# Performance work log

Hardware: AMD Instinct MI355X
Metric: run time of the kernel (lower is better)

The kernel has to match this reference:

```python
import jax, jax.numpy as jnp
import numpy as np

B, DIM, HEADS, HD, H, W = 1, 256, 8, 32, 64, 64
MLP = int(DIM * 4.0)
EPS = 1e-5


def _ln(x, g, b):
    # LayerNorm over channel dim of NCHW (torch applies it on NHWC last dim)
    mu = x.mean(axis=1, keepdims=True)
    var = ((x - mu) ** 2).mean(axis=1, keepdims=True)
    return (x - mu) / jnp.sqrt(var + EPS) * g[None, :, None, None] + b[None, :, None, None]


def _c1(x, w, b):
    # 1x1 conv: w is [out, in]
    return jnp.einsum('bchw,oc->bohw', x, w) + b[None, :, None, None]


def _c3(x, w, b):
    y = jax.lax.conv_general_dilated(x, w, (1, 1), ((1, 1), (1, 1)),
                                     dimension_numbers=('NCHW', 'OIHW', 'NCHW'))
    return y + b[None, :, None, None]


def setup_inputs() -> dict:
    key = jax.random.key(0)
    ks = jax.random.split(key, 16)
    init = lambda k, s: jax.random.normal(k, s, jnp.float32) * 0.02
    d = {}
    d['rgb_feat'] = jax.random.normal(ks[0], (B, DIM, H, W), jnp.float32)
    d['dpt_feat'] = jax.random.normal(ks[1], (B, DIM, H, W), jnp.float32)
    d['x_dpt'] = jax.random.normal(ks[2], (B, 1, 1024, 1024), jnp.float32)
    d['wq'] = init(ks[3], (DIM, DIM)); d['bq'] = jnp.zeros((DIM,), jnp.float32)
    d['wk'] = init(ks[4], (DIM, DIM)); d['bk'] = jnp.zeros((DIM,), jnp.float32)
    d['wv'] = init(ks[5], (DIM, DIM)); d['bv'] = jnp.zeros((DIM,), jnp.float32)
    d['wo'] = init(ks[6], (DIM, DIM)); d['bo'] = jnp.zeros((DIM,), jnp.float32)
    d['g_rgb'] = jnp.ones((DIM,), jnp.float32); d['b_rgb'] = jnp.zeros((DIM,), jnp.float32)
    d['g_dpt'] = jnp.ones((DIM,), jnp.float32); d['b_dpt'] = jnp.zeros((DIM,), jnp.float32)
    d['g1'] = jnp.ones((DIM,), jnp.float32); d['b1'] = jnp.zeros((DIM,), jnp.float32)
    d['g2'] = jnp.ones((DIM,), jnp.float32); d['b2'] = jnp.zeros((DIM,), jnp.float32)
    d['w_mlp1'] = init(ks[7], (MLP, DIM)); d['b_mlp1'] = jnp.zeros((MLP,), jnp.float32)
    d['w_mlp2'] = init(ks[8], (DIM, MLP)); d['b_mlp2'] = jnp.zeros((DIM,), jnp.float32)
    d['w_de1'] = init(ks[9], (DIM, 1, 3, 3)); d['b_de1'] = jnp.zeros((DIM,), jnp.float32)
    d['w_de2'] = init(ks[10], (DIM, DIM)); d['b_de2'] = jnp.zeros((DIM,), jnp.float32)
    d['pos_emb'] = init(ks[11], (1, DIM, 1, 1))
    d['scale'] = jnp.sqrt(jnp.float32(HD))
    return d


def reference(rgb_feat, dpt_feat, x_dpt, wq, bq, wk, bk, wv, bv, wo, bo,
              g_rgb, b_rgb, g_dpt, b_dpt, g1, b1, g2, b2,
              w_mlp1, b_mlp1, w_mlp2, b_mlp2, w_de1, b_de1, w_de2, b_de2,
              pos_emb, scale):
    Bn, C, Hh, Ww = rgb_feat.shape
    n = Hh * Ww
    rgb_ln = _ln(rgb_feat, g_rgb, b_rgb)
    dpt_ln = _ln(dpt_feat, g_dpt, b_dpt)
    # depth positional embedding: bilinear downsample (align_corners=False) + conv3x3 + relu + conv1x1
    xd = jax.image.resize(x_dpt, (Bn, 1, Hh, Ww), method='bilinear', antialias=False)
    pe = _c1(jax.nn.relu(_c3(xd, w_de1, b_de1)), w_de2, b_de2)
    rgb_ln = rgb_ln + pos_emb + pe
    dpt_ln = dpt_ln + pos_emb + pe
    # QKV as [B, heads, head_dim, N]
    q = _c1(rgb_ln, wq, bq).reshape(Bn, HEADS, HD, n)
    k = _c1(dpt_ln, wk, bk).reshape(Bn, HEADS, HD, n)
    v = _c1(dpt_ln, wv, bv).reshape(Bn, HEADS, HD, n)
    scores = jnp.einsum('bhdn,bhdm->bhnm', q, k) / scale
    attn = jax.nn.softmax(scores, axis=-1)  # dropout is identity in eval
    fused = jnp.einsum('bhnm,bhdm->bhdn', attn, v).reshape(Bn, C, Hh, Ww)
    out = _c1(fused, wo, bo) + rgb_feat
    out_ln = _ln(out, g1, b1)
    h = jax.nn.gelu(_c1(out_ln, w_mlp1, b_mlp1), approximate=False)
    mlp_out = _c1(h, w_mlp2, b_mlp2)
    out2 = mlp_out + out_ln
    return _ln(out2, g2, b2)
```

## Files before the change

kernel.cpp:

```cpp
#include <hip/hip_runtime.h>
#include <hip/hip_bf16.h>
#include <math.h>

constexpr int NTOK = 4096;
constexpr int CDIM = 256;
constexpr int MLPD = 1024;
constexpr int SPLIT = 4;
constexpr float EPS_LN = 1e-5f;

typedef __attribute__((ext_vector_type(8))) short bf16x8;
typedef __attribute__((ext_vector_type(4))) float floatx4;
typedef unsigned short u16;
typedef unsigned int u32;

__device__ __forceinline__ u16 f2bf(float x) {
    union { float f; u32 u; } v; v.f = x;
    u32 r = v.u + 0x7fff + ((v.u >> 16) & 1);
    return (u16)(r >> 16);
}
__device__ __forceinline__ float bf2f(u16 u) {
    union { u32 i; float f; } v; v.i = ((u32)u) << 16; return v.f;
}
__device__ __forceinline__ u32 pkbf(float a, float b) {
    __hip_bfloat162 h = __float22bfloat162_rn(make_float2(a, b));
    union { __hip_bfloat162 h; u32 u; } v; v.h = h; return v.u;
}
__device__ __forceinline__ float gelu_exact(float x) {
    return 0.5f * x * (1.0f + erff(x * 0.70710678118654752f));
}

__global__ __launch_bounds__(256) void k_prep(const float* __restrict__ rgb,
                                              float* __restrict__ rgbT,
                                              const float* __restrict__ dpt,
                                              float* __restrict__ dptT,
                                              const float* __restrict__ xdpt,
                                              const float* __restrict__ w3,
                                              const float* __restrict__ b3,
                                              u16* __restrict__ y,
                                              const float* __restrict__ wq,
                                              const float* __restrict__ wk,
                                              const float* __restrict__ wv,
                                              const float* __restrict__ wo,
                                              const float* __restrict__ wde2,
                                              const float* __restrict__ wm1,
                                              const float* __restrict__ wm2,
                                              u16* __restrict__ arena) {
    int blk = blockIdx.x;
    int t = threadIdx.x;
    if (blk < 512) {
        const float* in = (blk < 256) ? rgb : dpt;
        float* out = (blk < 256) ? rgbT : dptT;
        int tb = blk & 255;
        int c0 = (tb & 63) * 64, r0 = (tb >> 6) * 64;
        __shared__ float T[64][65];
        int rr = t >> 4, cc = (t & 15) * 4;
#pragma unroll
        for (int i = 0; i < 4; ++i) {
            int row = i * 16 + rr;
            float4 v = *(const float4*)(in + (size_t)(r0 + row) * NTOK + c0 + cc);
            T[row][cc] = v.x; T[row][cc + 1] = v.y; T[row][cc + 2] = v.z; T[row][cc + 3] = v.w;
        }
        __syncthreads();
#pragma unroll
        for (int i = 0; i < 4; ++i) {
            int a = i * 16 + rr;
            float4 v;
            v.x = T[cc][a]; v.y = T[cc + 1][a]; v.z = T[cc + 2][a]; v.w = T[cc + 3][a];
            *(float4*)(out + (size_t)(c0 + a) * CDIM + r0 + cc) = v;
        }
    } else if (blk < 768) {
        __shared__ float nb[3][18];
        int n0 = (blk - 512) * 16;
        int yy = n0 >> 6, x0 = n0 & 63;
        if (t < 54) {
            int r = t / 18, cc = t % 18;
            int sy = yy - 1 + r, sx = x0 - 1 + cc;
            float v = 0.f;
            if (sy >= 0 && sy < 64 && sx >= 0 && sx < 64) {
                int r0 = 16 * sy + 7, c0 = 16 * sx + 7;
                v = 0.25f * (xdpt[r0 * 1024 + c0] + xdpt[r0 * 1024 + c0 + 1] +
                             xdpt[(r0 + 1) * 1024 + c0] + xdpt[(r0 + 1) * 1024 + c0 + 1]);
            }
            nb[r][cc] = v;
        }
        __syncthreads();
        float wv9[9];
#pragma unroll
        for (int i = 0; i < 9; ++i) wv9[i] = w3[t * 9 + i];
        float bb = b3[t];
#pragma unroll
        for (int k = 0; k < 16; ++k) {
            float acc = bb;
#pragma unroll
            for (int r = 0; r < 3; ++r)
#pragma unroll
                for (int kx = 0; kx < 3; ++kx) acc += wv9[r * 3 + kx] * nb[r][k + kx];
            y[(size_t)(n0 + k) * CDIM + t] = f2bf(fmaxf(acc, 0.f));
        }
    } else {
        int e0 = (blk - 768) * 1024 + t * 4;
        const float* src; int off;
        if (e0 < 65536)       { src = wq;   off = 0; }
        else if (e0 < 131072) { src = wk;   off = 65536; }
        else if (e0 < 196608) { src = wv;   off = 131072; }
        else if (e0 < 262144) { src = wo;   off = 196608; }
        else if (e0 < 327680) { src = wde2; off = 262144; }
        else if (e0 < 589824) { src = wm1;  off = 327680; }
        else                  { src = wm2;  off = 589824; }
        float4 v = *(const float4*)(src + (e0 - off));
        uint2 o; o.x = pkbf(v.x, v.y); o.y = pkbf(v.z, v.w);
        *(uint2*)(arena + e0) = o;
    }
}

__global__ __launch_bounds__(256) void k_lnT(const void* __restrict__ xA,
                                             const float* __restrict__ gA,
                                             const float* __restrict__ bA,
                                             void* __restrict__ yA,
                                             const void* __restrict__ xB,
                                             const float* __restrict__ gB,
                                             const float* __restrict__ bB,
                                             void* __restrict__ yB,
                                             const u16* __restrict__ pe,
                                             const float* __restrict__ pos,
                                             int xf32) {
    const void* x; const float* g; const float* bb; void* y;
    if (blockIdx.y == 0) { x = xA; g = gA; bb = bA; y = yA; }
    else                 { x = xB; g = gB; bb = bB; y = yB; }
    int n = blockIdx.x * 4 + (threadIdx.x >> 6);
    int lane = threadIdx.x & 63;
    int c = lane * 4;
    float4 xv;
    if (xf32) {
        xv = *((const float4*)x + (size_t)n * 64 + lane);
    } else {
        ushort4 u = *((const ushort4*)x + (size_t)n * 64 + lane);
        xv = make_float4(bf2f(u.x), bf2f(u.y), bf2f(u.z), bf2f(u.w));
    }
    float s = xv.x + xv.y + xv.z + xv.w;
    float s2 = xv.x * xv.x + xv.y * xv.y + xv.z * xv.z + xv.w * xv.w;
#pragma unroll
    for (int off = 1; off < 64; off <<= 1) {
        s += __shfl_xor(s, off, 64);
        s2 += __shfl_xor(s2, off, 64);
    }
    float mu = s * (1.0f / 256.0f);
    float var = s2 * (1.0f / 256.0f) - mu * mu;
    float rsd = rsqrtf(var + EPS_LN);
    float4 g4 = *(const float4*)(g + c);
    float4 b4 = *(const float4*)(bb + c);
    float4 o;
    o.x = (xv.x - mu) * rsd * g4.x + b4.x;
    o.y = (xv.y - mu) * rsd * g4.y + b4.y;
    o.z = (xv.z - mu) * rsd * g4.z + b4.z;
    o.w = (xv.w - mu) * rsd * g4.w + b4.w;
    if (pe) {
        float4 p4 = *(const float4*)(pos + c);
        ushort4 pu = *((const ushort4*)pe + (size_t)n * 64 + lane);
        o.x += p4.x + bf2f(pu.x);
        o.y += p4.y + bf2f(pu.y);
        o.z += p4.z + bf2f(pu.z);
        o.w += p4.w + bf2f(pu.w);
    }
    ushort4 ou;
    ou.x = f2bf(o.x); ou.y = f2bf(o.y); ou.z = f2bf(o.z); ou.w = f2bf(o.w);
    *((ushort4*)y + (size_t)n * 64 + lane) = ou;
}

#define LDB 72
__global__ __launch_bounds__(512) void k_bmm(const u16* __restrict__ X0, const void* __restrict__ W0,
                                             const float* __restrict__ B0, void* __restrict__ Y0, int f0,
                                             const u16* __restrict__ X1, const void* __restrict__ W1,
                                             const float* __restrict__ B1, void* __restrict__ Y1, int f1,
                                             const u16* __restrict__ X2, const void* __restrict__ W2,
                                             const float* __restrict__ B2, void* __restrict__ Y2, int f2,
                                             const void* __restrict__ res, const float* __restrict__ scl,
                                             int M, int K) {
    const u16* X; const void* Wp; const float* bias; void* Yp; int flags;
    if (blockIdx.z == 0)      { X = X0; Wp = W0; bias = B0; Yp = Y0; flags = f0; }
    else if (blockIdx.z == 1) { X = X1; Wp = W1; bias = B1; Yp = Y1; flags = f1; }
    else                      { X = X2; Wp = W2; bias = B2; Yp = Y2; flags = f2; }
    __shared__ u16 Xs[2][64 * LDB];
    __shared__ u16 Ws[2][64 * LDB];
    float* Cred = (float*)&Xs[0][0];

    int tid = threadIdx.x;
    int kg = tid >> 8;
    int t = tid & 255;
    int wid = t >> 6, lane = t & 63;
    int lo16 = lane & 15, quad = lane >> 4;
    int wy = wid & 1, wx = wid >> 1;
    int n0 = blockIdx.x * 64, m0 = blockIdx.y * 64;
    int srow = t >> 2, sseg = t & 3;
    int Khalf = K >> 1;
    int kbase = kg * Khalf;

    floatx4 acc[2][2];
#pragma unroll
    for (int i = 0; i < 2; ++i)
#pragma unroll
        for (int j = 0; j < 2; ++j) acc[i][j] = floatx4{0.f, 0.f, 0.f, 0.f};

    for (int k0 = 0; k0 < Khalf; k0 += 64) {
        int kk = kbase + k0;
        const u16* xp = X + (size_t)(n0 + srow) * K + kk + sseg * 16;
        uint4 xr0 = *(const uint4*)xp;
        uint4 xr1 = *(const uint4*)(xp + 8);
        uint4 wb0, wb1;
        if (flags & 32) {
            const u16* wp = (const u16*)Wp + (size_t)(m0 + srow) * K + kk + sseg * 16;
            wb0 = *(const uint4*)wp;
            wb1 = *(const uint4*)(wp + 8);
        } else {
            const float* wp = (const float*)Wp + (size_t)(m0 + srow) * K + kk + sseg * 16;
            float4 w0 = *(const float4*)wp;
            float4 w1 = *(const float4*)(wp + 4);
            float4 w2 = *(const float4*)(wp + 8);
            float4 w3 = *(const float4*)(wp + 12);
            wb0.x = pkbf(w0.x, w0.y); wb0.y = pkbf(w0.z, w0.w);
            wb0.z = pkbf(w1.x, w1.y); wb0.w = pkbf(w1.z, w1.w);
            wb1.x = pkbf(w2.x, w2.y); wb1.y = pkbf(w2.z, w2.w);
            wb1.z = pkbf(w3.x, w3.y); wb1.w = pkbf(w3.z, w3.w);
        }
        __syncthreads();
        *(uint4*)&Xs[kg][srow * LDB + sseg * 16] = xr0;
        *(uint4*)&Xs[kg][srow * LDB + sseg * 16 + 8] = xr1;
        *(uint4*)&Ws[kg][srow * LDB + sseg * 16] = wb0;
        *(uint4*)&Ws[kg][srow * LDB + sseg * 16 + 8] = wb1;
        __syncthreads();

        const u16* As = (flags & 2) ? &Ws[kg][0] : &Xs[kg][0];
        const u16* Bs = (flags & 2) ? &Xs[kg][0] : &Ws[kg][0];
#pragma unroll
        for (int h = 0; h < 2; ++h) {
            int ko = h * 32 + quad * 8;
            bf16x8 a0 = *(const bf16x8*)&As[(wy * 32 + lo16) * LDB + ko];
            bf16x8 a1 = *(const bf16x8*)&As[(wy * 32 + 16 + lo16) * LDB + ko];
            bf16x8 b0 = *(const bf16x8*)&Bs[(wx * 32 + lo16) * LDB + ko];
            bf16x8 b1 = *(const bf16x8*)&Bs[(wx * 32 + 16 + lo16) * LDB + ko];
            acc[0][0] = __builtin_amdgcn_mfma_f32_16x16x32_bf16(a0, b0, acc[0][0], 0, 0, 0);
            acc[0][1] = __builtin_amdgcn_mfma_f32_16x16x32_bf16(a0, b1, acc[0][1], 0, 0, 0);
            acc[1][0] = __builtin_amdgcn_mfma_f32_16x16x32_bf16(a1, b0, acc[1][0], 0, 0, 0);
            acc[1][1] = __builtin_amdgcn_mfma_f32_16x16x32_bf16(a1, b1, acc[1][1], 0, 0, 0);
        }
    }

    __syncthreads();
    if (kg == 1) {
        float* c = &Cred[t * 17];
#pragma unroll
        for (int i = 0; i < 2; ++i)
#pragma unroll
            for (int j = 0; j < 2; ++j)
#pragma unroll
                for (int r = 0; r < 4; ++r) c[(i * 2 + j) * 4 + r] = acc[i][j][r];
    }
    __syncthreads();
    if (kg == 1) return;
    {
        const float* c = &Cred[t * 17];
#pragma unroll
        for (int i = 0; i < 2; ++i)
#pragma unroll
            for (int j = 0; j < 2; ++j)
#pragma unroll
                for (int r = 0; r < 4; ++r) acc[i][j][r] += c[(i * 2 + j) * 4 + r];
    }

    u16* Y = (u16*)Yp;
    if (flags & 2) {
#pragma unroll
        for (int i = 0; i < 2; ++i)
#pragma unroll
            for (int r = 0; r < 4; ++r) {
                int ch = m0 + wy * 32 + i * 16 + quad * 4 + r;
                float bb = bias[ch];
#pragma unroll
                for (int j = 0; j < 2; ++j) {
                    int tok = n0 + wx * 32 + j * 16 + lo16;
                    Y[(size_t)ch * NTOK + tok] = f2bf(acc[i][j][r] + bb);
                }
            }
    } else {
        float smul = (flags & 16) ? 1.4426950408889634f / scl[0] : 1.0f;
        float bj0 = bias[m0 + wx * 32 + lo16];
        float bj1 = bias[m0 + wx * 32 + 16 + lo16];
        const float* rf = (const float*)res;
        const u16* rb = (const u16*)res;
#pragma unroll
        for (int i = 0; i < 2; ++i)
#pragma unroll
            for (int j = 0; j < 2; ++j) {
                int ch = m0 + wx * 32 + j * 16 + lo16;
                float bb = j ? bj1 : bj0;
#pragma unroll
                for (int r = 0; r < 4; ++r) {
                    int tok = n0 + wy * 32 + i * 16 + quad * 4 + r;
                    float v = (acc[i][j][r] + bb) * smul;
                    if (flags & 1) v = gelu_exact(v);
                    if (flags & 4) v += rf[(size_t)tok * M + ch];
                    if (flags & 8) v += bf2f(rb[(size_t)tok * M + ch]);
                    if (flags & 64)
                        Y[((size_t)(ch >> 5) * NTOK + tok) * 32 + (ch & 31)] = f2bf(v);
                    else
                        Y[(size_t)tok * M + ch] = f2bf(v);
                }
            }
    }
}

#define LDK 40
#define LDV 72
__global__ __launch_bounds__(512) void k_fattn(const u16* __restrict__ Qh,
                                               const u16* __restrict__ Kh,
                                               const u16* __restrict__ Vc,
                                               u16* __restrict__ Op,
                                               float* __restrict__ Lp) {
    __shared__ u16 Kt[64 * LDK];
    __shared__ u16 Vt[32 * LDV];
    __shared__ u16 Pt[8][2][16 * LDV];

    int h = blockIdx.y;
    int q0 = blockIdx.x * 128;
    int sp = blockIdx.z;
    int tid = threadIdx.x;
    int wid = tid >> 6, lane = tid & 63;
    int lo16 = lane & 15, quad = lane >> 4;

    bf16x8 bq = *(const bf16x8*)(Qh + ((size_t)h * NTOK + q0 + wid * 16 + lo16) * 32 + quad * 8);

    int krow = tid >> 3, kseg = tid & 7;
    int vrow = tid >> 4, vseg = tid & 15;
    int kbase = sp * (NTOK / SPLIT);

    floatx4 o0 = {0.f, 0.f, 0.f, 0.f};
    floatx4 o1 = {0.f, 0.f, 0.f, 0.f};
    float lc[4] = {0.f, 0.f, 0.f, 0.f};

    for (int kt = 0; kt < NTOK / SPLIT / 64; ++kt) {
        int k0 = kbase + kt * 64;
        uint2 kreg = *(const uint2*)(Kh + ((size_t)h * NTOK + k0 + krow) * 32 + kseg * 4);
        uint2 vreg = *(const uint2*)(Vc + (size_t)(h * 32 + vrow) * NTOK + k0 + vseg * 4);
        __syncthreads();
        *(uint2*)&Kt[krow * LDK + kseg * 4] = kreg;
        *(uint2*)&Vt[vrow * LDV + vseg * 4] = vreg;
        __syncthreads();

        floatx4 s[4];
        floatx4 z = {0.f, 0.f, 0.f, 0.f};
#pragma unroll
        for (int c = 0; c < 4; ++c) {
            bf16x8 ak = *(const bf16x8*)&Kt[(c * 16 + lo16) * LDK + quad * 8];
            s[c] = __builtin_amdgcn_mfma_f32_16x16x32_bf16(ak, bq, z, 0, 0, 0);
        }
#pragma unroll
        for (int c = 0; c < 4; ++c) {
#pragma unroll
            for (int r = 0; r < 4; ++r) {
                float p = __builtin_amdgcn_exp2f(s[c][r]);
                s[c][r] = p;
                lc[c] += p;
            }
        }
        u16* P = &Pt[wid][kt & 1][0];
#pragma unroll
        for (int c = 0; c < 4; ++c) {
            uint2 w;
            w.x = pkbf(s[c][0], s[c][1]);
            w.y = pkbf(s[c][2], s[c][3]);
            *(uint2*)&P[lo16 * LDV + c * 16 + quad * 4] = w;
        }
#pragma unroll
        for (int kc = 0; kc < 2; ++kc) {
            bf16x8 bp = *(const bf16x8*)&P[lo16 * LDV + kc * 32 + quad * 8];
            bf16x8 av0 = *(const bf16x8*)&Vt[lo16 * LDV + kc * 32 + quad * 8];
            bf16x8 av1 = *(const bf16x8*)&Vt[(16 + lo16) * LDV + kc * 32 + quad * 8];
            o0 = __builtin_amdgcn_mfma_f32_16x16x32_bf16(av0, bp, o0, 0, 0, 0);
            o1 = __builtin_amdgcn_mfma_f32_16x16x32_bf16(av1, bp, o1, 0, 0, 0);
        }
    }

    float l = (lc[0] + lc[1]) + (lc[2] + lc[3]);
    l += __shfl_xor(l, 16, 64);
    l += __shfl_xor(l, 32, 64);

    size_t tok = q0 + wid * 16 + lo16;
    size_t obase = ((size_t)(sp * 8 + h) * NTOK + tok) * 32;
    uint2 w0; w0.x = pkbf(o0[0], o0[1]); w0.y = pkbf(o0[2], o0[3]);
    *(uint2*)(Op + obase + quad * 4) = w0;
    uint2 w1; w1.x = pkbf(o1[0], o1[1]); w1.y = pkbf(o1[2], o1[3]);
    *(uint2*)(Op + obase + 16 + quad * 4) = w1;
    if (quad == 0) Lp[(size_t)(sp * 8 + h) * NTOK + tok] = l;
}

__global__ __launch_bounds__(256) void k_comb(const u16* __restrict__ Op,
                                              const float* __restrict__ Lp,
                                              u16* __restrict__ fused) {
    int n = blockIdx.x * 4 + (threadIdx.x >> 6);
    int lane = threadIdx.x & 63;
    int c = lane * 4;
    int h = c >> 5, d = c & 31;
    float4 o = {0.f, 0.f, 0.f, 0.f};
    float l = 0.f;
#pragma unroll
    for (int s = 0; s < SPLIT; ++s) {
        size_t base = ((size_t)(s * 8 + h) * NTOK + n) * 32 + d;
        uint2 u = *(const uint2*)(Op + base);
        o.x += bf2f((u16)(u.x & 0xffff)); o.y += bf2f((u16)(u.x >> 16));
        o.z += bf2f((u16)(u.y & 0xffff)); o.w += bf2f((u16)(u.y >> 16));
        l += Lp[(size_t)(s * 8 + h) * NTOK + n];
    }
    float inv = 1.0f / l;
    uint2 w;
    w.x = pkbf(o.x * inv, o.y * inv);
    w.y = pkbf(o.z * inv, o.w * inv);
    *(uint2*)(fused + (size_t)n * CDIM + c) = w;
}

__global__ __launch_bounds__(256) void k_lntr(const u16* __restrict__ x,
                                              const float* __restrict__ g,
                                              const float* __restrict__ b,
                                              float* __restrict__ out) {
    __shared__ float T[16][260];
    int n0 = blockIdx.x * 16;
    int t = threadIdx.x;
    int tk = t >> 4, seg = t & 15;
    float v[16];
    {
        const u16* p = x + (size_t)(n0 + tk) * CDIM + seg * 16;
        uint4 a = *(const uint4*)p;
        uint4 bq = *(const uint4*)(p + 8);
        u32 uu[8] = {a.x, a.y, a.z, a.w, bq.x, bq.y, bq.z, bq.w};
#pragma unroll
        for (int i = 0; i < 8; ++i) {
            v[2 * i] = bf2f((u16)(uu[i] & 0xffff));
            v[2 * i + 1] = bf2f((u16)(uu[i] >> 16));
        }
    }
    float s = 0.f, s2 = 0.f;
#pragma unroll
    for (int i = 0; i < 16; ++i) { s += v[i]; s2 += v[i] * v[i]; }
#pragma unroll
    for (int off = 1; off < 16; off <<= 1) {
        s += __shfl_xor(s, off, 64);
        s2 += __shfl_xor(s2, off, 64);
    }
    float mu = s * (1.0f / 256.0f);
    float var = s2 * (1.0f / 256.0f) - mu * mu;
    float rsd = rsqrtf(var + EPS_LN);
#pragma unroll
    for (int i = 0; i < 16; ++i) {
        int c = seg * 16 + i;
        T[tk][c] = (v[i] - mu) * rsd * g[c] + b[c];
    }
    __syncthreads();
    int c = t;
    float o[16];
#pragma unroll
    for (int j = 0; j < 16; ++j) o[j] = T[j][c];
    float* dst = out + (size_t)c * NTOK + n0;
#pragma unroll
    for (int j = 0; j < 4; ++j) {
        float4 w = {o[4 * j], o[4 * j + 1], o[4 * j + 2], o[4 * j + 3]};
        *(float4*)(dst + 4 * j) = w;
    }
}

extern "C" void kernel_launch(void* const* d_in, const int* in_sizes, int n_in,
                              void* d_out, int out_size, void* d_ws, size_t ws_size,
                              hipStream_t stream) {
    const float* rgb    = (const float*)d_in[0];
    const float* dpt    = (const float*)d_in[1];
    const float* x_dpt  = (const float*)d_in[2];
    const float* wq     = (const float*)d_in[3];
    const float* bq     = (const float*)d_in[4];
    const float* wk     = (const float*)d_in[5];
    const float* bk     = (const float*)d_in[6];
    const float* wv     = (const float*)d_in[7];
    const float* bv     = (const float*)d_in[8];
    const float* wo     = (const float*)d_in[9];
    const float* bo     = (const float*)d_in[10];
    const float* g_rgb  = (const float*)d_in[11];
    const float* b_rgb  = (const float*)d_in[12];
    const float* g_dpt  = (const float*)d_in[13];
    const float* b_dpt  = (const float*)d_in[14];
    const float* g1     = (const float*)d_in[15];
    const float* b1     = (const float*)d_in[16];
    const float* g2     = (const float*)d_in[17];
    const float* b2     = (const float*)d_in[18];
    const float* w_mlp1 = (const float*)d_in[19];
    const float* b_mlp1 = (const float*)d_in[20];
    const float* w_mlp2 = (const float*)d_in[21];
    const float* b_mlp2 = (const float*)d_in[22];
    const float* w_de1  = (const float*)d_in[23];
    const float* b_de1  = (const float*)d_in[24];
    const float* w_de2  = (const float*)d_in[25];
    const float* b_de2  = (const float*)d_in[26];
    const float* pos    = (const float*)d_in[27];
    const float* scale  = (const float*)d_in[28];
    float* out = (float*)d_out;

    char* base = (char*)d_ws;
    const size_t MB = 1u << 20;
    float* rgbT    = (float*)(base + 0 * MB);
    float* dptT    = (float*)(base + 4 * MB);
    u16*   outT    = (u16*)(base + 4 * MB);
    float* Lp      = (float*)(base + 6 * MB);
    u16*   out_lnT = (u16*)(base + 6 * MB);
    u16*   relu3T  = (u16*)(base + 8 * MB);
    u16*   Op      = (u16*)(base + 8 * MB);
    u16*   hT      = (u16*)(base + 8 * MB);
    u16*   peT     = (u16*)(base + 10 * MB);
    u16*   aqT     = (u16*)(base + 12 * MB);
    u16*   akvT    = (u16*)(base + 14 * MB);
    u16*   Qhm     = (u16*)(base + 16 * MB);
    u16*   out2T   = (u16*)(base + 16 * MB);
    u16*   Khm     = (u16*)(base + 18 * MB);
    u16*   Vcm     = (u16*)(base + 20 * MB);
    u16*   fusedT  = (u16*)(base + 22 * MB);
    u16*   arena   = (u16*)(base + 24 * MB);

    bool aw = ws_size >= 26 * MB;
    int wf = aw ? 32 : 0;
    const void* Wq  = aw ? (const void*)(arena + 0)      : (const void*)wq;
    const void* Wk  = aw ? (const void*)(arena + 65536)  : (const void*)wk;
    const void* Wv  = aw ? (const void*)(arena + 131072) : (const void*)wv;
    const void* Wo  = aw ? (const void*)(arena + 196608) : (const void*)wo;
    const void* Wd2 = aw ? (const void*)(arena + 262144) : (const void*)w_de2;
    const void* Wm1 = aw ? (const void*)(arena + 327680) : (const void*)w_mlp1;
    const void* Wm2 = aw ? (const void*)(arena + 589824) : (const void*)w_mlp2;

    k_prep<<<aw ? 512 + 256 + 832 : 512 + 256, 256, 0, stream>>>(
        rgb, rgbT, dpt, dptT, x_dpt, w_de1, b_de1, relu3T,
        wq, wk, wv, wo, w_de2, w_mlp1, w_mlp2, arena);
    k_bmm<<<dim3(64, 4, 1), 512, 0, stream>>>(relu3T, Wd2, b_de2, peT, wf,
                                              nullptr, nullptr, nullptr, nullptr, 0,
                                              nullptr, nullptr, nullptr, nullptr, 0,
                                              nullptr, nullptr, CDIM, CDIM);
    k_lnT<<<dim3(1024, 2), 256, 0, stream>>>(rgbT, g_rgb, b_rgb, aqT,
                                             dptT, g_dpt, b_dpt, akvT,
                                             peT, pos, 1);
    k_bmm<<<dim3(64, 4, 3), 512, 0, stream>>>(aqT, Wq, bq, Qhm, wf | 16 | 64,
                                              akvT, Wk, bk, Khm, wf | 64,
                                              akvT, Wv, bv, Vcm, wf | 2,
                                              nullptr, scale, CDIM, CDIM);
    k_fattn<<<dim3(32, 8, SPLIT), 512, 0, stream>>>(Qhm, Khm, Vcm, Op, Lp);
    k_comb<<<1024, 256, 0, stream>>>(Op, Lp, fusedT);
    k_bmm<<<dim3(64, 4, 1), 512, 0, stream>>>(fusedT, Wo, bo, outT, wf | 4,
                                              nullptr, nullptr, nullptr, nullptr, 0,
                                              nullptr, nullptr, nullptr, nullptr, 0,
                                              rgbT, nullptr, CDIM, CDIM);
    k_lnT<<<dim3(1024, 1), 256, 0, stream>>>(outT, g1, b1, out_lnT,
                                             nullptr, nullptr, nullptr, nullptr,
                                             nullptr, nullptr, 0);
    k_bmm<<<dim3(64, 16, 1), 512, 0, stream>>>(out_lnT, Wm1, b_mlp1, hT, wf | 1,
                                               nullptr, nullptr, nullptr, nullptr, 0,
                                               nullptr, nullptr, nullptr, nullptr, 0,
                                               nullptr, nullptr, MLPD, CDIM);
    k_bmm<<<dim3(64, 4, 1), 512, 0, stream>>>(hT, Wm2, b_mlp2, out2T, wf | 8,
                                              nullptr, nullptr, nullptr, nullptr, 0,
                                              nullptr, nullptr, nullptr, nullptr, 0,
                                              out_lnT, nullptr, CDIM, MLPD);
    k_lntr<<<256, 256, 0, stream>>>(out2T, g2, b2, out);
}
```

Before: 217.8 us.

## Rewrite flash attention with 32x32 MFMA, register P exchange, and prefetched K/V

The attention kernel moves from 16x16x32 to 32x32x16 bf16 MFMA tiles. Each of 4 waves now handles 32 queries instead of each of 8 waves handling 16. The P tile is rebuilt in registers with a cross-lane shuffle instead of a round trip through shared memory. The next K/V tile is prefetched into registers with wider 16-byte loads while the current tile is computed. The aim is to cut LDS traffic and barriers per FLOP, at the cost of halving threads per block, which adds register pressure and may lower occupancy and the number of waves per CU.

```diff
diff --git a/kernel.cpp b/kernel.cpp
--- a/kernel.cpp
+++ b/kernel.cpp
@@ -10,6 +10,7 @@
 
 typedef __attribute__((ext_vector_type(8))) short bf16x8;
 typedef __attribute__((ext_vector_type(4))) float floatx4;
+typedef __attribute__((ext_vector_type(16))) float f32x16;
 typedef unsigned short u16;
 typedef unsigned int u32;
 
@@ -311,86 +312,93 @@
 
 #define LDK 40
 #define LDV 72
-__global__ __launch_bounds__(512) void k_fattn(const u16* __restrict__ Qh,
+__global__ __launch_bounds__(256) void k_fattn(const u16* __restrict__ Qh,
                                                const u16* __restrict__ Kh,
                                                const u16* __restrict__ Vc,
                                                u16* __restrict__ Op,
                                                float* __restrict__ Lp) {
     __shared__ u16 Kt[64 * LDK];
     __shared__ u16 Vt[32 * LDV];
-    __shared__ u16 Pt[8][2][16 * LDV];
 
     int h = blockIdx.y;
     int q0 = blockIdx.x * 128;
     int sp = blockIdx.z;
     int tid = threadIdx.x;
     int wid = tid >> 6, lane = tid & 63;
-    int lo16 = lane & 15, quad = lane >> 4;
-
-    bf16x8 bq = *(const bf16x8*)(Qh + ((size_t)h * NTOK + q0 + wid * 16 + lo16) * 32 + quad * 8);
-
-    int krow = tid >> 3, kseg = tid & 7;
-    int vrow = tid >> 4, vseg = tid & 15;
+    int ql = lane & 31, hi = lane >> 5;
+    int qtok = q0 + wid * 32 + ql;
+
+    bf16x8 bq0 = *(const bf16x8*)(Qh + ((size_t)h * NTOK + qtok) * 32 + hi * 8);
+    bf16x8 bq1 = *(const bf16x8*)(Qh + ((size_t)h * NTOK + qtok) * 32 + 16 + hi * 8);
+
+    int krow = tid >> 2, kseg = tid & 3;
+    int vrow = tid >> 3, vseg = tid & 7;
     int kbase = sp * (NTOK / SPLIT);
-
-    floatx4 o0 = {0.f, 0.f, 0.f, 0.f};
-    floatx4 o1 = {0.f, 0.f, 0.f, 0.f};
-    float lc[4] = {0.f, 0.f, 0.f, 0.f};
-
-    for (int kt = 0; kt < NTOK / SPLIT / 64; ++kt) {
-        int k0 = kbase + kt * 64;
-        uint2 kreg = *(const uint2*)(Kh + ((size_t)h * NTOK + k0 + krow) * 32 + kseg * 4);
-        uint2 vreg = *(const uint2*)(Vc + (size_t)(h * 32 + vrow) * NTOK + k0 + vseg * 4);
+    const int NITER = NTOK / SPLIT / 64;
+
+    f32x16 oacc = {0.f, 0.f, 0.f, 0.f, 0.f, 0.f, 0.f, 0.f,
+                   0.f, 0.f, 0.f, 0.f, 0.f, 0.f, 0.f, 0.f};
+    float l = 0.f;
+
+    uint4 kreg = *(const uint4*)(Kh + ((size_t)h * NTOK + kbase + krow) * 32 + kseg * 8);
+    uint4 vreg = *(const uint4*)(Vc + (size_t)(h * 32 + vrow) * NTOK + kbase + vseg * 8);
+
+    for (int kt = 0; kt < NITER; ++kt) {
         __syncthreads();
-        *(uint2*)&Kt[krow * LDK + kseg * 4] = kreg;
-        *(uint2*)&Vt[vrow * LDV + vseg * 4] = vreg;
+        *(uint4*)&Kt[krow * LDK + kseg * 8] = kreg;
+        *(uint4*)&Vt[vrow * LDV + vseg * 8] = vreg;
         __syncthreads();
-
-        floatx4 s[4];
-        floatx4 z = {0.f, 0.f, 0.f, 0.f};
-#pragma unroll
-        for (int c = 0; c < 4; ++c) {
-            bf16x8 ak = *(const bf16x8*)&Kt[(c * 16 + lo16) * LDK + quad * 8];
-            s[c] = __builtin_amdgcn_mfma_f32_16x16x32_bf16(ak, bq, z, 0, 0, 0);
-        }
-#pragma unroll
-        for (int c = 0; c < 4; ++c) {
-#pragma unroll
-            for (int r = 0; r < 4; ++r) {
-                float p = __builtin_amdgcn_exp2f(s[c][r]);
-                s[c][r] = p;
-                lc[c] += p;
+        if (kt + 1 < NITER) {
+            int kn = kbase + (kt + 1) * 64;
+            kreg = *(const uint4*)(Kh + ((size_t)h * NTOK + kn + krow) * 32 + kseg * 8);
+            vreg = *(const uint4*)(Vc + (size_t)(h * 32 + vrow) * NTOK + kn + vseg * 8);
+        }
+
+#pragma unroll
+        for (int sub = 0; sub < 2; ++sub) {
+            f32x16 s = {0.f, 0.f, 0.f, 0.f, 0.f, 0.f, 0.f, 0.f,
+                        0.f, 0.f, 0.f, 0.f, 0.f, 0.f, 0.f, 0.f};
+            bf16x8 ak0 = *(const bf16x8*)&Kt[(sub * 32 + ql) * LDK + hi * 8];
+            bf16x8 ak1 = *(const bf16x8*)&Kt[(sub * 32 + ql) * LDK + 16 + hi * 8];
+            s = __builtin_amdgcn_mfma_f32_32x32x16_bf16(ak0, bq0, s, 0, 0, 0);
+            s = __builtin_amdgcn_mfma_f32_32x32x16_bf16(ak1, bq1, s, 0, 0, 0);
+            u32 u[8], px[8];
+#pragma unroll
+            for (int t = 0; t < 8; ++t) {
+                float pa = __builtin_amdgcn_exp2f(s[2 * t]);
+                float pb = __builtin_amdgcn_exp2f(s[2 * t + 1]);
+                l += pa + pb;
+                u[t] = pkbf(pa, pb);
             }
-        }
-        u16* P = &Pt[wid][kt & 1][0];
-#pragma unroll
-        for (int c = 0; c < 4; ++c) {
-            uint2 w;
-            w.x = pkbf(s[c][0], s[c][1]);
-            w.y = pkbf(s[c][2], s[c][3]);
-            *(uint2*)&P[lo16 * LDV + c * 16 + quad * 4] = w;
-        }
-#pragma unroll
-        for (int kc = 0; kc < 2; ++kc) {
-            bf16x8 bp = *(const bf16x8*)&P[lo16 * LDV + kc * 32 + quad * 8];
-            bf16x8 av0 = *(const bf16x8*)&Vt[lo16 * LDV + kc * 32 + quad * 8];
-            bf16x8 av1 = *(const bf16x8*)&Vt[(16 + lo16) * LDV + kc * 32 + quad * 8];
-            o0 = __builtin_amdgcn_mfma_f32_16x16x32_bf16(av0, bp, o0, 0, 0, 0);
-            o1 = __builtin_amdgcn_mfma_f32_16x16x32_bf16(av1, bp, o1, 0, 0, 0);
-        }
-    }
-
-    float l = (lc[0] + lc[1]) + (lc[2] + lc[3]);
-    l += __shfl_xor(l, 16, 64);
+#pragma unroll
+            for (int t = 0; t < 8; ++t) px[t] = (u32)__shfl_xor((int)u[t], 32, 64);
+            uint4 wa, wb;
+            wa.x = hi ? px[2] : u[0];
+            wa.y = hi ? px[3] : u[1];
+            wa.z = hi ? u[2] : px[0];
+            wa.w = hi ? u[3] : px[1];
+            wb.x = hi ? px[6] : u[4];
+            wb.y = hi ? px[7] : u[5];
+            wb.z = hi ? u[6] : px[4];
+            wb.w = hi ? u[7] : px[5];
+            union { uint4 q; bf16x8 v; } pa0, pa1;
+            pa0.q = wa; pa1.q = wb;
+            bf16x8 bv0 = *(const bf16x8*)&Vt[ql * LDV + sub * 32 + hi * 8];
+            bf16x8 bv1 = *(const bf16x8*)&Vt[ql * LDV + sub * 32 + 16 + hi * 8];
+            oacc = __builtin_amdgcn_mfma_f32_32x32x16_bf16(pa0.v, bv0, oacc, 0, 0, 0);
+            oacc = __builtin_amdgcn_mfma_f32_32x32x16_bf16(pa1.v, bv1, oacc, 0, 0, 0);
+        }
+    }
+
     l += __shfl_xor(l, 32, 64);
 
-    size_t tok = q0 + wid * 16 + lo16;
-    size_t obase = ((size_t)(sp * 8 + h) * NTOK + tok) * 32;
-    uint2 w0; w0.x = pkbf(o0[0], o0[1]); w0.y = pkbf(o0[2], o0[3]);
-    *(uint2*)(Op + obase + quad * 4) = w0;
-    uint2 w1; w1.x = pkbf(o1[0], o1[1]); w1.y = pkbf(o1[2], o1[3]);
-    *(uint2*)(Op + obase + 16 + quad * 4) = w1;
-    if (quad == 0) Lp[(size_t)(sp * 8 + h) * NTOK + tok] = l;
+    size_t obase = ((size_t)(sp * 8 + h) * NTOK + q0 + wid * 32) * 32 + ql;
+#pragma unroll
+    for (int r = 0; r < 16; ++r) {
+        int qrow = (r & 3) + 8 * (r >> 2) + 4 * hi;
+        Op[obase + (size_t)qrow * 32] = f2bf(oacc[r]);
+    }
+    if (hi == 0) Lp[(size_t)(sp * 8 + h) * NTOK + qtok] = l;
 }
 
 __global__ __launch_bounds__(256) void k_comb(const u16* __restrict__ Op,
@@ -544,7 +552,7 @@
                                               akvT, Wk, bk, Khm, wf | 64,
                                               akvT, Wv, bv, Vcm, wf | 2,
                                               nullptr, scale, CDIM, CDIM);
-    k_fattn<<<dim3(32, 8, SPLIT), 512, 0, stream>>>(Qhm, Khm, Vcm, Op, Lp);
+    k_fattn<<<dim3(32, 8, SPLIT), 256, 0, stream>>>(Qhm, Khm, Vcm, Op, Lp);
     k_comb<<<1024, 256, 0, stream>>>(Op, Lp, fusedT);
     k_bmm<<<dim3(64, 4, 1), 512, 0, stream>>>(fusedT, Wo, bo, outT, wf | 4,
                                               nullptr, nullptr, nullptr, nullptr, 0,
```

After: 215.7 us. About the same (-0.9%).
